# Kernel optimization log

Hardware: AMD Instinct MI355X
Metric: run time of the kernel (lower is better)

## Reference

```python
import jax, jax.numpy as jnp
import numpy as np

D_MODEL = 1024
N_HEADS = 16
D_K = D_MODEL // N_HEADS
B, S = 4, 2048


def setup_inputs() -> dict:
    key = jax.random.key(0)
    ks = jax.random.split(key, 12)
    scale = 1.0 / np.sqrt(D_MODEL)
    mk = lambda k: (jax.random.uniform(k, (D_MODEL, D_MODEL), jnp.float32, -scale, scale))
    mb = lambda k: (jax.random.uniform(k, (D_MODEL,), jnp.float32, -scale, scale))
    mask = jnp.tril(jnp.ones((S, S), dtype=bool))[None, None, :, :]  # [1,1,S,S] causal
    return {
        "query": jax.random.normal(ks[0], (B, S, D_MODEL), jnp.float32),
        "key": jax.random.normal(ks[1], (B, S, D_MODEL), jnp.float32),
        "value": jax.random.normal(ks[2], (B, S, D_MODEL), jnp.float32),
        "w_q": mk(ks[3]), "b_q": mb(ks[4]),
        "w_k": mk(ks[5]), "b_k": mb(ks[6]),
        "w_v": mk(ks[7]), "b_v": mb(ks[8]),
        "w_o": mk(ks[9]), "b_o": mb(ks[10]),
        "mask": mask,
    }


def _split_heads(x):
    b, s, _ = x.shape
    return x.reshape(b, s, N_HEADS, D_K).transpose(0, 2, 1, 3)  # [B,H,S,Dk]


def reference(query, key, value, w_q, b_q, w_k, b_k, w_v, b_v, w_o, b_o, mask):
    Q = _split_heads(query @ w_q.T + b_q)
    K = _split_heads(key @ w_k.T + b_k)
    V = _split_heads(value @ w_v.T + b_v)
    scores = jnp.einsum("bhqd,bhkd->bhqk", Q, K) / jnp.sqrt(jnp.asarray(D_K, Q.dtype))
    min_val = jnp.finfo(scores.dtype).min
    scores = jnp.where(mask, scores, min_val)
    attn = jax.nn.softmax(scores, axis=-1)
    ctx = jnp.einsum("bhqk,bhkd->bhqd", attn, V)
    ctx = ctx.transpose(0, 2, 1, 3).reshape(query.shape[0], -1, D_MODEL)
    return ctx @ w_o.T + b_o
```

## Files before the change

kernel.cpp:

```cpp
#include <hip/hip_runtime.h>
#include <cstdint>
#include <cstddef>

#define DM 1024
#define NH 16
#define DK 64
#define BB 4
#define SS 2048
#define MROWS (BB*SS)

#define NE_ ((size_t)MROWS * DM)
#define WE_ ((size_t)DM * DM)

typedef __attribute__((ext_vector_type(8))) __bf16 bf16x8;
typedef __attribute__((ext_vector_type(4))) float f32x4;
typedef __attribute__((ext_vector_type(8))) unsigned short ushort8;

#define SCALE_LOG2E 0.18033688011112042f

__device__ __forceinline__ unsigned short f2bf(float f) {
  union { float f; unsigned u; } v; v.f = f;
  unsigned r = v.u + 0x7fffu + ((v.u >> 16) & 1u);
  return (unsigned short)(r >> 16);
}

__device__ __forceinline__ unsigned short f2bf_hw(float f) {
  __bf16 h = (__bf16)f;
  return __builtin_bit_cast(unsigned short, h);
}

__device__ __forceinline__ void async_load16(const void* g, void* l) {
  __builtin_amdgcn_global_load_lds(
      (__attribute__((address_space(1))) void*)(g),
      (__attribute__((address_space(3))) void*)(l),
      16, 0, 0);
}

template<int CTRL>
__device__ __forceinline__ float dppf(float v) {
  int i = __builtin_bit_cast(int, v);
  int r = __builtin_amdgcn_update_dpp(i, i, CTRL, 0xf, 0xf, true);
  return __builtin_bit_cast(float, r);
}
__device__ __forceinline__ float redsum16(float v) {
  v += dppf<0x128>(v);
  v += dppf<0x124>(v);
  v += dppf<0x122>(v);
  v += dppf<0x121>(v);
  return v;
}

struct CvtArgs {
  const float* src[7];
  unsigned short* dst[7];
};

__global__ __launch_bounds__(256)
void cvt_all(CvtArgs a) {
  size_t i = ((size_t)blockIdx.x * 256 + threadIdx.x) * 4;
  int seg; size_t off;
  if (i < 3 * NE_) { seg = (int)(i >> 23); off = i & (NE_ - 1); }
  else { size_t j = i - 3 * NE_; seg = 3 + (int)(j >> 20); off = j & (WE_ - 1); }
  float4 v = *reinterpret_cast<const float4*>(a.src[seg] + off);
  ushort4 o;
  o.x = f2bf(v.x); o.y = f2bf(v.y); o.z = f2bf(v.z); o.w = f2bf(v.w);
  *reinterpret_cast<ushort4*>(a.dst[seg] + off) = o;
}

#define GSTAGE(B, K0) { \
    _Pragma("unroll") \
    for (int p_ = 0; p_ < 2; ++p_) { \
      int idx_ = (p_ * 256 + tid) * 8; \
      int row_ = idx_ >> 5; \
      int sc_  = ((tid & 3) ^ ((row_ >> 1) & 3)) * 8; \
      async_load16(&A [(size_t)(gm0 + row_) * DM + (K0) + sc_], &As[B][idx_]); \
      async_load16(&Bw[(size_t)(gn0 + row_) * DM + (K0) + sc_], &Bs[B][idx_]); \
    } }

#define GCOMPUTE(BUF) { \
    bf16x8 af[4], bfr[4]; \
    _Pragma("unroll") \
    for (int m_ = 0; m_ < 4; ++m_) { \
      int row_ = wm*64 + m_*16 + lrow; \
      af[m_] = *reinterpret_cast<const bf16x8*>(&As[BUF][row_*32 + ((kg ^ ((row_>>1)&3)))*8]); \
    } \
    _Pragma("unroll") \
    for (int n_ = 0; n_ < 4; ++n_) { \
      int row_ = wn*64 + n_*16 + lrow; \
      bfr[n_] = *reinterpret_cast<const bf16x8*>(&Bs[BUF][row_*32 + ((kg ^ ((row_>>1)&3)))*8]); \
    } \
    __builtin_amdgcn_s_setprio(1); \
    _Pragma("unroll") \
    for (int m_ = 0; m_ < 4; ++m_) \
      _Pragma("unroll") \
      for (int n_ = 0; n_ < 4; ++n_) \
        acc[m_][n_] = __builtin_amdgcn_mfma_f32_16x16x32_bf16(af[m_], bfr[n_], acc[m_][n_], 0, 0, 0); \
    __builtin_amdgcn_s_setprio(0); \
  }

#define GKLOOP() \
  GSTAGE(0, 0); \
  GSTAGE(1, 32); \
  for (int kt = 0; kt < 31; ++kt) { \
    asm volatile("s_waitcnt vmcnt(4)" ::: "memory"); \
    __builtin_amdgcn_s_barrier(); \
    __builtin_amdgcn_sched_barrier(0); \
    if (kt + 2 < 32) { GSTAGE((kt + 2) % 3, (kt + 2) * 32); } \
    GCOMPUTE(kt % 3); \
  } \
  asm volatile("s_waitcnt vmcnt(0)" ::: "memory"); \
  __builtin_amdgcn_s_barrier(); \
  __builtin_amdgcn_sched_barrier(0); \
  GCOMPUTE(1);

struct QkvArgs {
  const unsigned short* A[3];
  const unsigned short* W[3];
  const float* bias[3];
  unsigned short* out[3];
};

__global__ __launch_bounds__(256)
void gemm_qkv(QkvArgs qa)
{
  __shared__ __align__(16) unsigned short As[3][128*32];
  __shared__ __align__(16) unsigned short Bs[3][128*32];

  int wgid = blockIdx.x + blockIdx.y * 24;
  wgid = (wgid & 7) * 192 + (wgid >> 3);
  const int bx = wgid % 24, by = wgid / 24;

  const int sel = bx >> 3;
  const unsigned short* __restrict__ A  = qa.A[sel];
  const unsigned short* __restrict__ Bw = qa.W[sel];
  const float* __restrict__ bias = qa.bias[sel];
  unsigned short* __restrict__ o = qa.out[sel];
  const float qs = (sel == 0) ? SCALE_LOG2E : 1.0f;

  const int tid  = threadIdx.x;
  const int lane = tid & 63;
  const int wv   = tid >> 6;
  const int wm   = wv >> 1, wn = wv & 1;
  const int gm0  = by * 128;
  const int gn0  = (bx & 7) * 128;
  const int lrow = lane & 15;
  const int kg   = lane >> 4;

  f32x4 acc[4][4] = {};

  GKLOOP();

  const int orow = (lane >> 4) * 4;
  const int ocol = lane & 15;
  #pragma unroll
  for (int n = 0; n < 4; ++n) {
    int gn = gn0 + wn*64 + n*16 + ocol;
    float bv = bias[gn] * qs;
    int h = gn >> 6, d = gn & (DK - 1);
    #pragma unroll
    for (int m = 0; m < 4; ++m) {
      #pragma unroll
      for (int r = 0; r < 4; ++r) {
        int gm = gm0 + wm*64 + m*16 + orow + r;
        int b = gm >> 11, s = gm & (SS - 1);
        o[(((size_t)b*NH + h)*SS + s)*DK + d] = f2bf_hw(fmaf(acc[m][n][r], qs, bv));
      }
    }
  }
}

__global__ __launch_bounds__(256)
void gemm_out(const unsigned short* __restrict__ A,
              const unsigned short* __restrict__ Bw,
              const float* __restrict__ bias,
              float* __restrict__ o)
{
  __shared__ __align__(16) unsigned short As[3][128*32];
  __shared__ __align__(16) unsigned short Bs[3][128*32];

  int wgid = blockIdx.x + blockIdx.y * 8;
  wgid = (wgid & 7) * 64 + (wgid >> 3);
  const int bx = wgid & 7, by = wgid >> 3;

  const int tid  = threadIdx.x;
  const int lane = tid & 63;
  const int wv   = tid >> 6;
  const int wm   = wv >> 1, wn = wv & 1;
  const int gm0  = by * 128;
  const int gn0  = bx * 128;
  const int lrow = lane & 15;
  const int kg   = lane >> 4;

  f32x4 acc[4][4] = {};

  GKLOOP();

  const int orow = (lane >> 4) * 4;
  const int ocol = lane & 15;
  #pragma unroll
  for (int n = 0; n < 4; ++n) {
    int gn = gn0 + wn*64 + n*16 + ocol;
    float bv = bias[gn];
    #pragma unroll
    for (int m = 0; m < 4; ++m)
      #pragma unroll
      for (int r = 0; r < 4; ++r) {
        int gm = gm0 + wm*64 + m*16 + orow + r;
        o[(size_t)gm * DM + gn] = acc[m][n][r] + bv;
      }
  }
}

__global__ __launch_bounds__(256)
void vtrans_kernel(const unsigned short* __restrict__ Vp, unsigned short* __restrict__ VpT) {
  __shared__ unsigned short T[64][72];
  const int bh = blockIdx.x;
  const int st = blockIdx.y;
  const int tid = threadIdx.x;
  #pragma unroll
  for (int p = 0; p < 2; ++p) {
    int i = p*256 + tid;
    int row = i >> 3, c8 = (i & 7) * 8;
    *reinterpret_cast<ushort8*>(&T[row][c8]) =
      *reinterpret_cast<const ushort8*>(&Vp[((size_t)bh*SS + st*64 + row)*DK + c8]);
  }
  __syncthreads();
  #pragma unroll
  for (int p = 0; p < 2; ++p) {
    int i = p*256 + tid;
    int d = i >> 3, s8 = (i & 7) * 8;
    ushort8 o;
    #pragma unroll
    for (int j = 0; j < 8; ++j) o[j] = T[s8 + j][d];
    *reinterpret_cast<ushort8*>(&VpT[((size_t)bh*DK + d)*SS + st*64 + s8]) = o;
  }
}

__global__ __launch_bounds__(512)
void attn_kernel(const unsigned short* __restrict__ Qp,
                 const unsigned short* __restrict__ Kp,
                 const unsigned short* __restrict__ VpT,
                 unsigned short* __restrict__ ctx)
{
  __shared__ __align__(16) unsigned short Kb[2][64*64];
  __shared__ __align__(16) unsigned short Vb[2][64*64];
  __shared__ __align__(16) unsigned short Ps[8][16][72];

  const int tid  = threadIdx.x;
  const int lane = tid & 63;
  const int w    = tid >> 6;
  const int bh   = blockIdx.x;
  const int qt   = gridDim.y - 1 - blockIdx.y;
  const int qb0  = qt * 128;
  const int qw0  = qb0 + w * 16;
  const int lrow = lane & 15;
  const int g0   = lane >> 4;
  const int lk8  = g0 * 8;

  const size_t qbase = ((size_t)bh * SS + qw0 + lrow) * DK;
  bf16x8 aq0 = *reinterpret_cast<const bf16x8*>(&Qp[qbase + lk8]);
  bf16x8 aq1 = *reinterpret_cast<const bf16x8*>(&Qp[qbase + 32 + lk8]);

  f32x4 accc[4] = {};
  float psum[4] = {0.f, 0.f, 0.f, 0.f};

  const int ntiles = 2*qt + 2;
  const int twlast = (qw0 + 15) >> 6;
  const int srow   = tid >> 3;
  const int ssrc   = (tid & 7) ^ (srow & 7);

#define STAGE(B, T) { \
    const int kv0_ = (T) * 64; \
    async_load16(&Kp [((size_t)bh*SS + kv0_ + srow)*DK + ssrc*8], &Kb[B][tid*8]); \
    async_load16(&VpT[((size_t)bh*DK + srow)*SS + kv0_ + ssrc*8], &Vb[B][tid*8]); }

  STAGE(0, 0);

  for (int t = 0; t < ntiles; ++t) {
    const int buf = t & 1;
    asm volatile("s_waitcnt vmcnt(0)" ::: "memory");
    __syncthreads();
    if (t + 1 < ntiles) { if (buf) { STAGE(0, t + 1); } else { STAGE(1, t + 1); } }

    if (t <= twlast) {
      const int kv0 = t * 64;
      const unsigned short* Kc = &Kb[buf][0];
      const unsigned short* Vc = &Vb[buf][0];

      f32x4 sc[4];
      __builtin_amdgcn_s_setprio(1);
      #pragma unroll
      for (int kb = 0; kb < 4; ++kb) {
        const int rk = kb*16 + lrow;
        const int cx = rk & 7;
        bf16x8 bk0 = *reinterpret_cast<const bf16x8*>(&Kc[rk*64 + ((g0    ) ^ cx)*8]);
        bf16x8 bk1 = *reinterpret_cast<const bf16x8*>(&Kc[rk*64 + ((g0 + 4) ^ cx)*8]);
        f32x4 z = {};
        z      = __builtin_amdgcn_mfma_f32_16x16x32_bf16(aq0, bk0, z, 0, 0, 0);
        sc[kb] = __builtin_amdgcn_mfma_f32_16x16x32_bf16(aq1, bk1, z, 0, 0, 0);
      }
      __builtin_amdgcn_s_setprio(0);

      const int qrow0 = qw0 + g0 * 4;
      const bool needmask = (kv0 + 63 > qw0);
      #pragma unroll
      for (int kb = 0; kb < 4; ++kb) {
        const int kvg = kv0 + kb*16 + lrow;
        #pragma unroll
        for (int r = 0; r < 4; ++r) {
          float p = __builtin_amdgcn_exp2f(sc[kb][r]);
          if (needmask && (kvg > qrow0 + r)) p = 0.f;
          sc[kb][r] = p;
          psum[r] += p;
        }
      }

      #pragma unroll
      for (int kb = 0; kb < 4; ++kb)
        #pragma unroll
        for (int r = 0; r < 4; ++r)
          Ps[w][g0*4 + r][kb*16 + lrow] = f2bf_hw(sc[kb][r]);
      asm volatile("s_waitcnt lgkmcnt(0)" ::: "memory");

      bf16x8 pa0 = *reinterpret_cast<const bf16x8*>(&Ps[w][lrow][lk8]);
      bf16x8 pa1 = *reinterpret_cast<const bf16x8*>(&Ps[w][lrow][32 + lk8]);
      __builtin_amdgcn_s_setprio(1);
      #pragma unroll
      for (int db = 0; db < 4; ++db) {
        const int rv = db*16 + lrow;
        const int cv = rv & 7;
        bf16x8 bv0 = *reinterpret_cast<const bf16x8*>(&Vc[rv*64 + ((g0    ) ^ cv)*8]);
        bf16x8 bv1 = *reinterpret_cast<const bf16x8*>(&Vc[rv*64 + ((g0 + 4) ^ cv)*8]);
        accc[db] = __builtin_amdgcn_mfma_f32_16x16x32_bf16(pa0, bv0, accc[db], 0, 0, 0);
        accc[db] = __builtin_amdgcn_mfma_f32_16x16x32_bf16(pa1, bv1, accc[db], 0, 0, 0);
      }
      __builtin_amdgcn_s_setprio(0);
    }
  }

  const int b = bh >> 4, hh = bh & (NH - 1);
  #pragma unroll
  for (int r = 0; r < 4; ++r) {
    int q = qw0 + g0*4 + r;
    float l = redsum16(psum[r]);
    float inv = __builtin_amdgcn_rcpf(l);
    size_t base = ((size_t)b * SS + q) * DM + hh * DK;
    #pragma unroll
    for (int db = 0; db < 4; ++db)
      ctx[base + db*16 + lrow] = f2bf_hw(accc[db][r] * inv);
  }
}

extern "C" void kernel_launch(void* const* d_in, const int* in_sizes, int n_in,
                              void* d_out, int out_size, void* d_ws, size_t ws_size,
                              hipStream_t stream)
{
  const float* q_in = (const float*)d_in[0];
  const float* k_in = (const float*)d_in[1];
  const float* v_in = (const float*)d_in[2];
  const float* w_q  = (const float*)d_in[3];
  const float* b_q  = (const float*)d_in[4];
  const float* w_k  = (const float*)d_in[5];
  const float* b_k  = (const float*)d_in[6];
  const float* w_v  = (const float*)d_in[7];
  const float* b_v  = (const float*)d_in[8];
  const float* w_o  = (const float*)d_in[9];
  const float* b_o  = (const float*)d_in[10];

  char* ws = (char*)d_ws;
  size_t off = 0;
  unsigned short* xb[3];
  unsigned short* wb[4];
  for (int i = 0; i < 3; ++i) { xb[i] = (unsigned short*)(ws + off); off += NE_ * 2; }
  for (int i = 0; i < 4; ++i) { wb[i] = (unsigned short*)(ws + off); off += WE_ * 2; }
  unsigned short* Qp  = (unsigned short*)(ws + off); off += NE_ * 2;
  unsigned short* Kp  = (unsigned short*)(ws + off); off += NE_ * 2;
  unsigned short* Vp  = (unsigned short*)(ws + off); off += NE_ * 2;
  unsigned short* ctx = (unsigned short*)(ws + off); off += NE_ * 2;
  unsigned short* VpT = xb[2];

  CvtArgs ca;
  ca.src[0] = q_in; ca.dst[0] = xb[0];
  ca.src[1] = k_in; ca.dst[1] = xb[1];
  ca.src[2] = v_in; ca.dst[2] = xb[2];
  ca.src[3] = w_q;  ca.dst[3] = wb[0];
  ca.src[4] = w_k;  ca.dst[4] = wb[1];
  ca.src[5] = w_v;  ca.dst[5] = wb[2];
  ca.src[6] = w_o;  ca.dst[6] = wb[3];
  const int cvt_blocks = (int)((3*NE_ + 4*WE_) / 1024);
  cvt_all<<<cvt_blocks, 256, 0, stream>>>(ca);

  QkvArgs qa;
  qa.A[0] = xb[0]; qa.W[0] = wb[0]; qa.bias[0] = b_q; qa.out[0] = Qp;
  qa.A[1] = xb[1]; qa.W[1] = wb[1]; qa.bias[1] = b_k; qa.out[1] = Kp;
  qa.A[2] = xb[2]; qa.W[2] = wb[2]; qa.bias[2] = b_v; qa.out[2] = Vp;
  gemm_qkv<<<dim3(24, MROWS/128), 256, 0, stream>>>(qa);

  vtrans_kernel<<<dim3(BB*NH, SS/64), 256, 0, stream>>>(Vp, VpT);

  attn_kernel<<<dim3(BB*NH, SS/128), 512, 0, stream>>>(Qp, Kp, VpT, ctx);

  gemm_out<<<dim3(DM/128, MROWS/128), 256, 0, stream>>>(ctx, wb[3], b_o, (float*)d_out);
}
```

Baseline: 187.5 us.

## Fuse fp32-to-bf16 activation conversion into QKV GEMM and write V transposed

The QKV GEMM now loads fp32 activations straight into registers, converts them to bf16 and writes them to LDS itself, so the separate pass that converted the three large activation tensors is gone and only the weights are still pre-converted. The V projection epilogue writes its output already transposed (head, d, s), which removes the vtrans kernel and its extra round trip through memory. The cost is that the A operand now goes through registers instead of async direct-to-LDS loads, reading twice the bytes per tile with more register pressure and a reworked wait/barrier pipeline. The transposed V stores are also narrower 8-byte writes.

```diff
diff --git a/kernel.cpp b/kernel.cpp
--- a/kernel.cpp
+++ b/kernel.cpp
@@ -51,30 +51,51 @@
 }
 
 struct CvtArgs {
-  const float* src[7];
-  unsigned short* dst[7];
+  const float* src[4];
+  unsigned short* dst[4];
 };
 
 __global__ __launch_bounds__(256)
 void cvt_all(CvtArgs a) {
   size_t i = ((size_t)blockIdx.x * 256 + threadIdx.x) * 4;
-  int seg; size_t off;
-  if (i < 3 * NE_) { seg = (int)(i >> 23); off = i & (NE_ - 1); }
-  else { size_t j = i - 3 * NE_; seg = 3 + (int)(j >> 20); off = j & (WE_ - 1); }
+  int seg = (int)(i >> 20);
+  size_t off = i & (WE_ - 1);
   float4 v = *reinterpret_cast<const float4*>(a.src[seg] + off);
   ushort4 o;
   o.x = f2bf(v.x); o.y = f2bf(v.y); o.z = f2bf(v.z); o.w = f2bf(v.w);
   *reinterpret_cast<ushort4*>(a.dst[seg] + off) = o;
 }
 
-#define GSTAGE(B, K0) { \
+struct QkvArgs {
+  const float* A[3];
+  const unsigned short* W[3];
+  const float* bias[3];
+  unsigned short* out[3];
+};
+
+#define GLOAD(B, K0, RL) { \
     _Pragma("unroll") \
     for (int p_ = 0; p_ < 2; ++p_) { \
       int idx_ = (p_ * 256 + tid) * 8; \
       int row_ = idx_ >> 5; \
       int sc_  = ((tid & 3) ^ ((row_ >> 1) & 3)) * 8; \
-      async_load16(&A [(size_t)(gm0 + row_) * DM + (K0) + sc_], &As[B][idx_]); \
+      const float* ap_ = &A[(size_t)(gm0 + row_) * DM + (K0) + sc_]; \
+      RL[p_][0] = *reinterpret_cast<const float4*>(ap_); \
+      RL[p_][1] = *reinterpret_cast<const float4*>(ap_ + 4); \
       async_load16(&Bw[(size_t)(gn0 + row_) * DM + (K0) + sc_], &Bs[B][idx_]); \
+    } }
+
+#define GWRITE(B, RW) { \
+    _Pragma("unroll") \
+    for (int p_ = 0; p_ < 2; ++p_) { \
+      int idx_ = (p_ * 256 + tid) * 8; \
+      ushort8 w_; \
+      _Pragma("unroll") \
+      for (int j_ = 0; j_ < 4; ++j_) { \
+        w_[j_]     = f2bf_hw(RW[p_][0][j_]); \
+        w_[4 + j_] = f2bf_hw(RW[p_][1][j_]); \
+      } \
+      *reinterpret_cast<ushort8*>(&As[B][idx_]) = w_; \
     } }
 
 #define GCOMPUTE(BUF) { \
@@ -98,27 +119,33 @@
     __builtin_amdgcn_s_setprio(0); \
   }
 
-#define GKLOOP() \
-  GSTAGE(0, 0); \
-  GSTAGE(1, 32); \
-  for (int kt = 0; kt < 31; ++kt) { \
-    asm volatile("s_waitcnt vmcnt(4)" ::: "memory"); \
+#define GITER(KT, RL, RW) { \
+    if ((KT) + 2 < 32) { GLOAD(((KT) + 2) % 3, ((KT) + 2) * 32, RL); } \
+    GCOMPUTE((KT) % 3); \
+    if ((KT) + 1 < 32) { \
+      if ((KT) + 2 < 32) { asm volatile("s_waitcnt vmcnt(6)" ::: "memory"); } \
+      else               { asm volatile("s_waitcnt vmcnt(0)" ::: "memory"); } \
+      GWRITE(((KT) + 1) % 3, RW); \
+    } \
+    asm volatile("s_waitcnt lgkmcnt(0)" ::: "memory"); \
     __builtin_amdgcn_s_barrier(); \
     __builtin_amdgcn_sched_barrier(0); \
-    if (kt + 2 < 32) { GSTAGE((kt + 2) % 3, (kt + 2) * 32); } \
-    GCOMPUTE(kt % 3); \
-  } \
-  asm volatile("s_waitcnt vmcnt(0)" ::: "memory"); \
-  __builtin_amdgcn_s_barrier(); \
-  __builtin_amdgcn_sched_barrier(0); \
-  GCOMPUTE(1);
-
-struct QkvArgs {
-  const unsigned short* A[3];
-  const unsigned short* W[3];
-  const float* bias[3];
-  unsigned short* out[3];
-};
+  }
+
+#define GKLOOP_F32A() { \
+    float4 ra0[2][2], ra1[2][2]; \
+    GLOAD(0, 0, ra0); \
+    GLOAD(1, 32, ra1); \
+    asm volatile("s_waitcnt vmcnt(6)" ::: "memory"); \
+    GWRITE(0, ra0); \
+    asm volatile("s_waitcnt lgkmcnt(0)" ::: "memory"); \
+    __builtin_amdgcn_s_barrier(); \
+    __builtin_amdgcn_sched_barrier(0); \
+    for (int kt = 0; kt < 32; kt += 2) { \
+      GITER(kt,     ra0, ra1); \
+      GITER(kt + 1, ra1, ra0); \
+    } \
+  }
 
 __global__ __launch_bounds__(256)
 void gemm_qkv(QkvArgs qa)
@@ -131,7 +158,7 @@
   const int bx = wgid % 24, by = wgid / 24;
 
   const int sel = bx >> 3;
-  const unsigned short* __restrict__ A  = qa.A[sel];
+  const float* __restrict__ A = qa.A[sel];
   const unsigned short* __restrict__ Bw = qa.W[sel];
   const float* __restrict__ bias = qa.bias[sel];
   unsigned short* __restrict__ o = qa.out[sel];
@@ -148,26 +175,56 @@
 
   f32x4 acc[4][4] = {};
 
-  GKLOOP();
+  GKLOOP_F32A();
 
   const int orow = (lane >> 4) * 4;
   const int ocol = lane & 15;
-  #pragma unroll
-  for (int n = 0; n < 4; ++n) {
-    int gn = gn0 + wn*64 + n*16 + ocol;
-    float bv = bias[gn] * qs;
-    int h = gn >> 6, d = gn & (DK - 1);
+  if (sel != 2) {
     #pragma unroll
-    for (int m = 0; m < 4; ++m) {
-      #pragma unroll
-      for (int r = 0; r < 4; ++r) {
-        int gm = gm0 + wm*64 + m*16 + orow + r;
-        int b = gm >> 11, s = gm & (SS - 1);
-        o[(((size_t)b*NH + h)*SS + s)*DK + d] = f2bf_hw(fmaf(acc[m][n][r], qs, bv));
+    for (int n = 0; n < 4; ++n) {
+      int gn = gn0 + wn*64 + n*16 + ocol;
+      float bv = bias[gn] * qs;
+      int h = gn >> 6, d = gn & (DK - 1);
+      #pragma unroll
+      for (int m = 0; m < 4; ++m) {
+        #pragma unroll
+        for (int r = 0; r < 4; ++r) {
+          int gm = gm0 + wm*64 + m*16 + orow + r;
+          int b = gm >> 11, s = gm & (SS - 1);
+          o[(((size_t)b*NH + h)*SS + s)*DK + d] = f2bf_hw(fmaf(acc[m][n][r], qs, bv));
+        }
       }
     }
-  }
-}
+  } else {
+    #pragma unroll
+    for (int n = 0; n < 4; ++n) {
+      int gn = gn0 + wn*64 + n*16 + ocol;
+      float bv = bias[gn];
+      int h = gn >> 6, d = gn & (DK - 1);
+      #pragma unroll
+      for (int m = 0; m < 4; ++m) {
+        int s0 = gm0 + wm*64 + m*16 + orow;
+        int b  = s0 >> 11, s = s0 & (SS - 1);
+        ushort4 w;
+        w.x = f2bf_hw(acc[m][n][0] + bv);
+        w.y = f2bf_hw(acc[m][n][1] + bv);
+        w.z = f2bf_hw(acc[m][n][2] + bv);
+        w.w = f2bf_hw(acc[m][n][3] + bv);
+        *reinterpret_cast<ushort4*>(&o[(((size_t)b*NH + h)*DK + d)*SS + s]) = w;
+      }
+    }
+  }
+}
+
+#define GSTAGE(B, K0) { \
+    _Pragma("unroll") \
+    for (int p_ = 0; p_ < 2; ++p_) { \
+      int idx_ = (p_ * 256 + tid) * 8; \
+      int row_ = idx_ >> 5; \
+      int sc_  = ((tid & 3) ^ ((row_ >> 1) & 3)) * 8; \
+      async_load16(&A [(size_t)(gm0 + row_) * DM + (K0) + sc_], &As[B][idx_]); \
+      async_load16(&Bw[(size_t)(gn0 + row_) * DM + (K0) + sc_], &Bs[B][idx_]); \
+    } }
 
 __global__ __launch_bounds__(256)
 void gemm_out(const unsigned short* __restrict__ A,
@@ -193,7 +250,19 @@
 
   f32x4 acc[4][4] = {};
 
-  GKLOOP();
+  GSTAGE(0, 0);
+  GSTAGE(1, 32);
+  for (int kt = 0; kt < 31; ++kt) {
+    asm volatile("s_waitcnt vmcnt(4)" ::: "memory");
+    __builtin_amdgcn_s_barrier();
+    __builtin_amdgcn_sched_barrier(0);
+    if (kt + 2 < 32) { GSTAGE((kt + 2) % 3, (kt + 2) * 32); }
+    GCOMPUTE(kt % 3);
+  }
+  asm volatile("s_waitcnt vmcnt(0)" ::: "memory");
+  __builtin_amdgcn_s_barrier();
+  __builtin_amdgcn_sched_barrier(0);
+  GCOMPUTE(1);
 
   const int orow = (lane >> 4) * 4;
   const int ocol = lane & 15;
@@ -208,31 +277,6 @@
         int gm = gm0 + wm*64 + m*16 + orow + r;
         o[(size_t)gm * DM + gn] = acc[m][n][r] + bv;
       }
-  }
-}
-
-__global__ __launch_bounds__(256)
-void vtrans_kernel(const unsigned short* __restrict__ Vp, unsigned short* __restrict__ VpT) {
-  __shared__ unsigned short T[64][72];
-  const int bh = blockIdx.x;
-  const int st = blockIdx.y;
-  const int tid = threadIdx.x;
-  #pragma unroll
-  for (int p = 0; p < 2; ++p) {
-    int i = p*256 + tid;
-    int row = i >> 3, c8 = (i & 7) * 8;
-    *reinterpret_cast<ushort8*>(&T[row][c8]) =
-      *reinterpret_cast<const ushort8*>(&Vp[((size_t)bh*SS + st*64 + row)*DK + c8]);
-  }
-  __syncthreads();
-  #pragma unroll
-  for (int p = 0; p < 2; ++p) {
-    int i = p*256 + tid;
-    int d = i >> 3, s8 = (i & 7) * 8;
-    ushort8 o;
-    #pragma unroll
-    for (int j = 0; j < 8; ++j) o[j] = T[s8 + j][d];
-    *reinterpret_cast<ushort8*>(&VpT[((size_t)bh*DK + d)*SS + st*64 + s8]) = o;
   }
 }
 
@@ -369,35 +413,26 @@
 
   char* ws = (char*)d_ws;
   size_t off = 0;
-  unsigned short* xb[3];
   unsigned short* wb[4];
-  for (int i = 0; i < 3; ++i) { xb[i] = (unsigned short*)(ws + off); off += NE_ * 2; }
   for (int i = 0; i < 4; ++i) { wb[i] = (unsigned short*)(ws + off); off += WE_ * 2; }
   unsigned short* Qp  = (unsigned short*)(ws + off); off += NE_ * 2;
   unsigned short* Kp  = (unsigned short*)(ws + off); off += NE_ * 2;
-  unsigned short* Vp  = (unsigned short*)(ws + off); off += NE_ * 2;
+  unsigned short* VpT = (unsigned short*)(ws + off); off += NE_ * 2;
   unsigned short* ctx = (unsigned short*)(ws + off); off += NE_ * 2;
-  unsigned short* VpT = xb[2];
 
   CvtArgs ca;
-  ca.src[0] = q_in; ca.dst[0] = xb[0];
-  ca.src[1] = k_in; ca.dst[1] = xb[1];
-  ca.src[2] = v_in; ca.dst[2] = xb[2];
-  ca.src[3] = w_q;  ca.dst[3] = wb[0];
-  ca.src[4] = w_k;  ca.dst[4] = wb[1];
-  ca.src[5] = w_v;  ca.dst[5] = wb[2];
-  ca.src[6] = w_o;  ca.dst[6] = wb[3];
-  const int cvt_blocks = (int)((3*NE_ + 4*WE_) / 1024);
-  cvt_all<<<cvt_blocks, 256, 0, stream>>>(ca);
+  ca.src[0] = w_q; ca.dst[0] = wb[0];
+  ca.src[1] = w_k; ca.dst[1] = wb[1];
+  ca.src[2] = w_v; ca.dst[2] = wb[2];
+  ca.src[3] = w_o; ca.dst[3] = wb[3];
+  cvt_all<<<(int)(4*WE_/1024), 256, 0, stream>>>(ca);
 
   QkvArgs qa;
-  qa.A[0] = xb[0]; qa.W[0] = wb[0]; qa.bias[0] = b_q; qa.out[0] = Qp;
-  qa.A[1] = xb[1]; qa.W[1] = wb[1]; qa.bias[1] = b_k; qa.out[1] = Kp;
-  qa.A[2] = xb[2]; qa.W[2] = wb[2]; qa.bias[2] = b_v; qa.out[2] = Vp;
+  qa.A[0] = q_in; qa.W[0] = wb[0]; qa.bias[0] = b_q; qa.out[0] = Qp;
+  qa.A[1] = k_in; qa.W[1] = wb[1]; qa.bias[1] = b_k; qa.out[1] = Kp;
+  qa.A[2] = v_in; qa.W[2] = wb[2]; qa.bias[2] = b_v; qa.out[2] = VpT;
   gemm_qkv<<<dim3(24, MROWS/128), 256, 0, stream>>>(qa);
 
-  vtrans_kernel<<<dim3(BB*NH, SS/64), 256, 0, stream>>>(Vp, VpT);
-
   attn_kernel<<<dim3(BB*NH, SS/128), 512, 0, stream>>>(Qp, Kp, VpT, ctx);
 
   gemm_out<<<dim3(DM/128, MROWS/128), 256, 0, stream>>>(ctx, wb[3], b_o, (float*)d_out);
```

Measured after the change: 175.9 us. 1.07x faster.
